# Kernel tuning notes

Hardware: AMD Instinct MI355X
Metric: run time of the kernel (lower is better)

The kernel has to match this reference:

```python
import jax, jax.numpy as jnp
import numpy as np

B, H, W = 8, 448, 448
HID, EMB, OUT = 1024, 1024, 4096
P = 12544
hgrid = wgrid = H // 14  # 32


def layernorm2d(x, wgt, bias, eps=1e-6):
    # channel-wise LN over dim 1 per spatial location, as in LayerNorm2d
    u = x.mean(1, keepdims=True)
    s = ((x - u) ** 2).mean(1, keepdims=True)
    x = (x - u) / jnp.sqrt(s + eps)
    return wgt[None, :, None, None] * x + bias[None, :, None, None]


def conv2d(x, wk, b, stride):
    y = jax.lax.conv_general_dilated(x, wk, (stride, stride), 'VALID',
                                     dimension_numbers=('NCHW', 'OIHW', 'NCHW'))
    return y + b[None, :, None, None]


def grid_sample_bilinear(feat, grid):
    # feat [B,C,h,w]; grid [B,P,2] (x,y) in [-1,1]; align_corners=False, zeros padding
    Bc, C, Hh, Ww = feat.shape
    gx = (grid[..., 0] + 1.0) * 0.5 * Ww - 0.5
    gy = (grid[..., 1] + 1.0) * 0.5 * Hh - 0.5
    x0 = jnp.floor(gx); y0 = jnp.floor(gy)
    x1 = x0 + 1.0; y1 = y0 + 1.0
    wx1 = gx - x0; wx0 = 1.0 - wx1
    wy1 = gy - y0; wy0 = 1.0 - wy1
    flat = feat.reshape(Bc, C, Hh * Ww)

    def gather(ix, iy):
        valid = (ix >= 0) & (ix < Ww) & (iy >= 0) & (iy < Hh)
        ixc = jnp.clip(ix, 0, Ww - 1).astype(jnp.int32)
        iyc = jnp.clip(iy, 0, Hh - 1).astype(jnp.int32)
        idx = iyc * Ww + ixc  # [B,P]
        g = jnp.take_along_axis(flat, idx[:, None, :], axis=2)  # [B,C,P]
        return g * valid[:, None, :].astype(g.dtype)

    return (gather(x0, y0) * (wx0 * wy0)[:, None, :]
            + gather(x1, y0) * (wx1 * wy0)[:, None, :]
            + gather(x0, y1) * (wx0 * wy1)[:, None, :]
            + gather(x1, y1) * (wx1 * wy1)[:, None, :])


def forward(images, masks, image_features, point_coords, valid_mask,
            c1w, c1b, ln1w, ln1b, c2w, c2b, ln2w, ln2b, c3w, c3b, up_w, up_b):
    x = jnp.concatenate([images, masks], axis=1)  # [B,4,H,W]
    x = conv2d(x, c1w, c1b, 7)
    x = jax.nn.gelu(layernorm2d(x, ln1w, ln1b), approximate=False)
    x = conv2d(x, c2w, c2b, 2)
    x = jax.nn.gelu(layernorm2d(x, ln2w, ln2b), approximate=False)
    x = conv2d(x, c3w, c3b, 1)  # [B,EMB,h,w]
    feat = image_features.reshape(B, hgrid, wgrid, EMB).transpose(0, 3, 1, 2)
    x = x + feat
    # point_sample: coords in [0,1], mapped to [-1,1]
    sf = grid_sample_bilinear(x, 2.0 * point_coords - 1.0)  # [B,EMB,P]
    sf = sf.transpose(0, 2, 1)  # [B,P,EMB]
    vm = valid_mask.astype(sf.dtype)
    pooled = (sf * vm[:, :, None]).sum(1) / vm.sum(1)[:, None]
    pooled = jnp.nan_to_num(pooled)
    out = pooled @ up_w.T + up_b  # [B,OUT]
    return out  # single feature level: stack([out]).mean(0) == out


def setup_inputs() -> dict:
    key = jax.random.key(0)
    ks = jax.random.split(key, 12)
    rng = np.random.default_rng(0)

    masks_np = np.zeros((B, 1, H, W), np.float32)
    coords = np.full((B, P, 2), -1.0, np.float32)
    valid = np.zeros((B, P), bool)
    for b in range(B):
        y0r = int(rng.integers(0, H // 2)); x0r = int(rng.integers(0, W // 2))
        hh = int(rng.integers(H // 4, H // 2)); ww = int(rng.integers(W // 4, W // 2))
        masks_np[b, 0, y0r:y0r + hh, x0r:x0r + ww] = 1.0
        ys, xs = np.nonzero(masks_np[b, 0])
        n = len(ys)
        sel = np.sort(rng.choice(n, size=min(P, n), replace=False))
        k = len(sel)
        coords[b, :k, 0] = xs[sel] / W  # x normalized (flip of (y,x))
        coords[b, :k, 1] = ys[sel] / H  # y normalized
        valid[b, :k] = True

    s = 0.02
    return {
        'images': jax.random.normal(ks[0], (B, 3, H, W), jnp.float32),
        'masks': jnp.asarray(masks_np),
        'image_features': jax.random.normal(ks[1], (B, hgrid * wgrid, EMB), jnp.float32),
        'point_coords': jnp.asarray(coords),
        'valid_mask': jnp.asarray(valid),
        'c1w': jax.random.normal(ks[2], (HID // 4, 4, 7, 7), jnp.float32) * s,
        'c1b': jnp.zeros((HID // 4,), jnp.float32),
        'ln1w': jnp.ones((HID // 4,), jnp.float32),
        'ln1b': jnp.zeros((HID // 4,), jnp.float32),
        'c2w': jax.random.normal(ks[3], (HID, HID // 4, 2, 2), jnp.float32) * s,
        'c2b': jnp.zeros((HID,), jnp.float32),
        'ln2w': jnp.ones((HID,), jnp.float32),
        'ln2b': jnp.zeros((HID,), jnp.float32),
        'c3w': jax.random.normal(ks[4], (EMB, HID, 1, 1), jnp.float32) * s,
        'c3b': jnp.zeros((EMB,), jnp.float32),
        'up_w': jax.random.normal(ks[5], (OUT, EMB), jnp.float32) * s,
        'up_b': jnp.zeros((OUT,), jnp.float32),
    }


def reference(images, masks, image_features, point_coords, valid_mask,
              c1w, c1b, ln1w, ln1b, c2w, c2b, ln2w, ln2b, c3w, c3b, up_w, up_b):
    return forward(images, masks, image_features, point_coords, valid_mask,
                   c1w, c1b, ln1w, ln1b, c2w, c2b, ln2w, ln2b, c3w, c3b, up_w, up_b)
```

## Files before the change

kernel.cpp:

```cpp
#include <hip/hip_runtime.h>
#include <stdint.h>

#define NB 8
#define HIN 448
#define CH1 256
#define CH2 1024
#define NLOC 1024
#define M2 8192
#define M1 32768
#define K1 224
#define NPTS 12544
#define NOUT 4096
#define CAP 384
#define MC (NB * CAP)
#define M1C (MC * 4)

typedef __attribute__((ext_vector_type(8))) short bf16x8;
typedef __attribute__((ext_vector_type(4))) float f32x4;

__device__ __forceinline__ short f2bf(float f) {
  uint32_t u = __builtin_bit_cast(uint32_t, f);
  uint32_t r = (u + 0x7fffu + ((u >> 16) & 1u)) >> 16;
  return (short)r;
}
__device__ __forceinline__ float bf2f(short s) {
  return __builtin_bit_cast(float, (uint32_t)(uint16_t)s << 16);
}
__device__ __forceinline__ float gelu_f(float x) {
  return 0.5f * x * (1.0f + erff(x * 0.70710678118654752f));
}
__device__ __forceinline__ void gload_lds16(const void* g, void* l) {
  __builtin_amdgcn_global_load_lds((const __attribute__((address_space(1))) unsigned int*)g,
                                   (__attribute__((address_space(3))) unsigned int*)l, 16, 0, 0);
}

__global__ void k_prep(const float* __restrict__ c1w, const float* __restrict__ c2w,
                       short* __restrict__ c1wb, short* __restrict__ w2p,
                       float4* __restrict__ zp, int n4) {
  int i = blockIdx.x * 256 + threadIdx.x;
  if (i < n4) zp[i] = make_float4(0.f, 0.f, 0.f, 0.f);
  if (i < CH1 * K1) {
    int o = i / K1, k = i - o * K1;
    int c = k / 56, kk = k - c * 56, r = kk >> 3, cc = kk & 7;
    c1wb[i] = f2bf(cc < 7 ? c1w[((o * 4 + c) * 7 + r) * 7 + cc] : 0.0f);
  }
  if (i < CH2 * CH2) {
    int o = i >> 10, k = i & 1023;
    int pos = k >> 8, ci = k & 255;
    w2p[i] = f2bf(c2w[(size_t)(o * 256 + ci) * 4 + pos]);
  }
}

__global__ __launch_bounds__(256) void k_pts(const float* __restrict__ coords,
                                             float* __restrict__ Aw,
                                             float* __restrict__ cnt,
                                             float* __restrict__ sumAw) {
  __shared__ float lAw[NLOC];
  __shared__ int lcnt;
  __shared__ float wsum[4];
  int t = threadIdx.x;
  int b = blockIdx.x / 49;
  int blk = blockIdx.x - b * 49;
  for (int i = t; i < NLOC; i += 256) lAw[i] = 0.f;
  if (t == 0) lcnt = 0;
  __syncthreads();
  int pi = blk * 256 + t;
  float x = coords[((size_t)b * NPTS + pi) * 2];
  float y = coords[((size_t)b * NPTS + pi) * 2 + 1];
  bool valid = (x >= 0.0f);
  if (valid) {
    float gx = x * 32.0f - 0.5f, gy = y * 32.0f - 0.5f;
    float x0f = floorf(gx), y0f = floorf(gy);
    int x0 = (int)x0f, y0 = (int)y0f;
    float wx1 = gx - x0f, wx0 = 1.0f - wx1;
    float wy1 = gy - y0f, wy0 = 1.0f - wy1;
    int xs[2] = {x0, x0 + 1}, ys[2] = {y0, y0 + 1};
    float wxs[2] = {wx0, wx1}, wys[2] = {wy0, wy1};
    #pragma unroll
    for (int cy = 0; cy < 2; cy++)
      #pragma unroll
      for (int cx = 0; cx < 2; cx++) {
        int ix = xs[cx], iy = ys[cy];
        if (ix >= 0 && ix < 32 && iy >= 0 && iy < 32)
          atomicAdd(&lAw[iy * 32 + ix], wxs[cx] * wys[cy]);
      }
  }
  unsigned long long ball = __ballot(valid);
  if ((t & 63) == 0) atomicAdd(&lcnt, (int)__popcll(ball));
  __syncthreads();
  float tsum = 0.f;
  for (int i = t; i < NLOC; i += 256) {
    float v = lAw[i];
    tsum += v;
    if (v != 0.f) atomicAdd(&Aw[b * NLOC + i], v);
  }
  #pragma unroll
  for (int m = 1; m <= 32; m <<= 1) tsum += __shfl_xor(tsum, m, 64);
  if ((t & 63) == 0) wsum[t >> 6] = tsum;
  __syncthreads();
  if (t == 0) {
    float bs = wsum[0] + wsum[1] + wsum[2] + wsum[3];
    if (bs != 0.f) atomicAdd(&sumAw[b], bs);
    if (lcnt) atomicAdd(&cnt[b], (float)lcnt);
  }
}

__global__ __launch_bounds__(256) void k_cim(const float* __restrict__ Aw,
                                             int* __restrict__ idxc,
                                             float* __restrict__ Awc,
                                             const float* __restrict__ images,
                                             const float* __restrict__ masks,
                                             short* __restrict__ A1g) {
  __shared__ float S[28 * 452];
  int t = threadIdx.x;
  if (blockIdx.x < NB) {
    int* cnts = (int*)S;
    int* offs = cnts + 256;
    int b = blockIdx.x;
    int base = b * 1024 + t * 4;
    float w[4];
    int c = 0;
    #pragma unroll
    for (int j = 0; j < 4; j++) { w[j] = Aw[base + j]; c += (w[j] != 0.f) ? 1 : 0; }
    cnts[t] = c;
    offs[t] = c;
    __syncthreads();
    for (int s = 1; s < 256; s <<= 1) {
      int v = (t >= s) ? offs[t - s] : 0;
      __syncthreads();
      offs[t] += v;
      __syncthreads();
    }
    int pos = b * CAP + offs[t] - cnts[t];
    int lim = (b + 1) * CAP;
    #pragma unroll
    for (int j = 0; j < 4; j++)
      if (w[j] != 0.f && pos < lim) { idxc[pos] = base + j; Awc[pos] = w[j]; pos++; }
    int total = offs[255];
    for (int i = total + t; i < CAP; i += 256) {
      idxc[b * CAP + i] = b * 1024;
      Awc[b * CAP + i] = 0.f;
    }
    return;
  }
  int bid = blockIdx.x - NB;
  int b = bid >> 6, y = bid & 63;
  int y7 = y * 7;
  for (int p = t; p < 3136; p += 256) {
    int row = p / 112, c4 = p - row * 112;
    int c = row / 7, r = row - c * 7;
    const float* src = (c < 3)
        ? &images[((size_t)(b * 3 + c) * 448 + y7 + r) * 448 + c4 * 4]
        : &masks[((size_t)b * 448 + y7 + r) * 448 + c4 * 4];
    *(float4*)&S[row * 452 + c4 * 4] = *(const float4*)src;
  }
  __syncthreads();
  size_t obase = (size_t)bid * 64 * K1;
  #pragma unroll
  for (int it = 0; it < 7; it++) {
    int p = it * 256 + t;
    int x = p / 28, k16 = p - x * 28;
    const float* s = &S[k16 * 452 + x * 7];
    short o[8];
    #pragma unroll
    for (int j = 0; j < 7; j++) o[j] = f2bf(s[j]);
    o[7] = 0;
    *(bf16x8*)&A1g[obase + (size_t)p * 8] = *(bf16x8*)o;
  }
}

template<int KDIM, int LDC, int MODE>
__global__ __launch_bounds__(256) void k_gemm64(
    const short* __restrict__ Amat, const int* __restrict__ idxc,
    const short* __restrict__ Bmat, const float* __restrict__ bias,
    short* __restrict__ Cout) {
  __shared__ __align__(16) char Lraw[16384];
  int t = threadIdx.x, lane = t & 63, wv = t >> 6;
  int mt0 = blockIdx.x * 64;
  int nt0 = blockIdx.y * 64;
  f32x4 acc[2][2];
  #pragma unroll
  for (int i = 0; i < 2; i++)
    #pragma unroll
    for (int j = 0; j < 2; j++) acc[i][j] = (f32x4){0.f, 0.f, 0.f, 0.f};

  int srow = lane >> 2, scol = (lane & 3) * 8;
  int wm = wv >> 1, wn = wv & 1;
  int l15 = lane & 15, lg = lane >> 4;

  int arow = mt0 + wv * 16 + srow;
  const short* Ap;
  if (MODE == 1) {
    int i = arow >> 2, pos = arow & 3;
    int loc = idxc[i];
    int b = loc >> 10, oy = (loc >> 5) & 31, ox = loc & 31;
    int yy = oy * 2 + (pos >> 1), xx = ox * 2 + (pos & 1);
    Ap = Amat + (size_t)((b * 64 + yy) * 64 + xx) * KDIM;
  } else {
    Ap = Amat + (size_t)arow * KDIM;
  }
  const short* Bp = Bmat + (size_t)(nt0 + wv * 16 + srow) * KDIM;

  auto STAGE = [&](int buf, int kt) {
    int k0 = kt * 32;
    char* As = Lraw + buf * 8192;
    char* Bs = As + 4096;
    gload_lds16(Ap + k0 + scol, As + wv * 1024);
    gload_lds16(Bp + k0 + scol, Bs + wv * 1024);
  };

  const int NT = KDIM / 32;
  STAGE(0, 0);
  __syncthreads();
  int cur = 0;
  #pragma unroll 2
  for (int kt = 0; kt < NT; kt++) {
    if (kt + 1 < NT) STAGE(cur ^ 1, kt + 1);
    const short* As = (const short*)(Lraw + cur * 8192);
    const short* Bs = As + 2048;
    bf16x8 af[2], bfr[2];
    #pragma unroll
    for (int i = 0; i < 2; i++)
      af[i] = *(const bf16x8*)&As[(wm * 32 + i * 16 + l15) * 32 + lg * 8];
    #pragma unroll
    for (int j = 0; j < 2; j++)
      bfr[j] = *(const bf16x8*)&Bs[(wn * 32 + j * 16 + l15) * 32 + lg * 8];
    #pragma unroll
    for (int i = 0; i < 2; i++)
      #pragma unroll
      for (int j = 0; j < 2; j++)
        acc[i][j] = __builtin_amdgcn_mfma_f32_16x16x32_bf16(af[i], bfr[j], acc[i][j], 0, 0, 0);
    __syncthreads();
    cur ^= 1;
  }

  short* ct = (short*)Lraw;
  #pragma unroll
  for (int i = 0; i < 2; i++)
    #pragma unroll
    for (int j = 0; j < 2; j++) {
      int cl = wn * 32 + j * 16 + l15;
      float bv = bias[nt0 + cl];
      #pragma unroll
      for (int reg = 0; reg < 4; reg++) {
        int rl = wm * 32 + i * 16 + lg * 4 + reg;
        ct[rl * 68 + cl] = f2bf(acc[i][j][reg] + bv);
      }
    }
  __syncthreads();
  #pragma unroll
  for (int it = 0; it < 2; it++) {
    int p = it * 256 + t;
    int row = p >> 3, cc = (p & 7) * 8;
    bf16x8 v = *(const bf16x8*)&ct[row * 68 + cc];
    *(bf16x8*)&Cout[(size_t)(mt0 + row) * LDC + nt0 + cc] = v;
  }
}

__global__ __launch_bounds__(256) void k_gemm2s(
    const short* __restrict__ Amat, const short* __restrict__ Bmat,
    const float* __restrict__ bias, float* __restrict__ y2p0,
    float* __restrict__ y2p1) {
  const int KDIM = 1024;
  __shared__ __align__(16) char Lraw[24576];
  int t = threadIdx.x, lane = t & 63, wv = t >> 6;
  int mt0 = blockIdx.x * 128;
  int nt0 = blockIdx.y * 64;
  int kz = blockIdx.z;
  int kbase = kz * 512;
  float* outp = kz ? y2p1 : y2p0;
  f32x4 acc[4][2];
  #pragma unroll
  for (int i = 0; i < 4; i++)
    #pragma unroll
    for (int j = 0; j < 2; j++) acc[i][j] = (f32x4){0.f, 0.f, 0.f, 0.f};

  int srow = lane >> 2, scol = (lane & 3) * 8;
  int wm = wv >> 1, wn = wv & 1;
  int l15 = lane & 15, lg = lane >> 4;
  int r0 = wv * 16, r1 = 64 + wv * 16;

  auto STAGE = [&](int buf, int kt) {
    int k0 = kbase + kt * 32;
    char* As = Lraw + buf * 12288;
    char* Bs = As + 8192;
    gload_lds16(&Amat[(size_t)(mt0 + r0 + srow) * KDIM + k0 + scol], As + r0 * 64);
    gload_lds16(&Amat[(size_t)(mt0 + r1 + srow) * KDIM + k0 + scol], As + r1 * 64);
    gload_lds16(&Bmat[(size_t)(nt0 + r0 + srow) * KDIM + k0 + scol], Bs + r0 * 64);
  };

  STAGE(0, 0);
  __syncthreads();
  int cur = 0;
  #pragma unroll 2
  for (int kt = 0; kt < 16; kt++) {
    if (kt + 1 < 16) STAGE(cur ^ 1, kt + 1);
    const short* As = (const short*)(Lraw + cur * 12288);
    const short* Bs = As + 4096;
    bf16x8 af[4], bfr[2];
    #pragma unroll
    for (int i = 0; i < 4; i++)
      af[i] = *(const bf16x8*)&As[(wm * 64 + i * 16 + l15) * 32 + lg * 8];
    #pragma unroll
    for (int j = 0; j < 2; j++)
      bfr[j] = *(const bf16x8*)&Bs[(wn * 32 + j * 16 + l15) * 32 + lg * 8];
    #pragma unroll
    for (int i = 0; i < 4; i++)
      #pragma unroll
      for (int j = 0; j < 2; j++)
        acc[i][j] = __builtin_amdgcn_mfma_f32_16x16x32_bf16(af[i], bfr[j], acc[i][j], 0, 0, 0);
    __syncthreads();
    cur ^= 1;
  }

  #pragma unroll
  for (int i = 0; i < 4; i++)
    #pragma unroll
    for (int j = 0; j < 2; j++) {
      int colg = nt0 + wn * 32 + j * 16 + l15;
      float bv = kz ? 0.0f : bias[colg];
      #pragma unroll
      for (int reg = 0; reg < 4; reg++) {
        int rowg = mt0 + wm * 64 + i * 16 + lg * 4 + reg;
        outp[(size_t)rowg * 1024 + colg] = acc[i][j][reg] + bv;
      }
    }
}

__global__ __launch_bounds__(256) void k_ln1c(const short* __restrict__ y1c,
                                              const float* __restrict__ ln1w,
                                              const float* __restrict__ ln1b,
                                              short* __restrict__ act1c) {
  int t = threadIdx.x, wv = t >> 6, lane = t & 63;
  int c = lane * 4;
  float lw[4], lb[4];
  #pragma unroll
  for (int j = 0; j < 4; j++) { lw[j] = ln1w[c + j]; lb[j] = ln1b[c + j]; }
  int j0 = blockIdx.x * 64 + wv * 16;
  for (int r = 0; r < 16; r++) {
    int j = j0 + r;
    short4 v4 = *(const short4*)&y1c[(size_t)j * 256 + c];
    float xs[4] = {bf2f(v4.x), bf2f(v4.y), bf2f(v4.z), bf2f(v4.w)};
    float s = 0.f, q = 0.f;
    #pragma unroll
    for (int jj = 0; jj < 4; jj++) { s += xs[jj]; q += xs[jj] * xs[jj]; }
    #pragma unroll
    for (int mm = 1; mm <= 32; mm <<= 1) { s += __shfl_xor(s, mm, 64); q += __shfl_xor(q, mm, 64); }
    float u = s * (1.0f / 256.0f);
    float rs = rsqrtf(q * (1.0f / 256.0f) - u * u + 1e-6f);
    short o[4];
    #pragma unroll
    for (int jj = 0; jj < 4; jj++) o[jj] = f2bf(gelu_f(lw[jj] * ((xs[jj] - u) * rs) + lb[jj]));
    *(short4*)&act1c[(size_t)j * 256 + c] = make_short4(o[0], o[1], o[2], o[3]);
  }
}

__global__ __launch_bounds__(256) void k_poolboth(
    const float* __restrict__ y2p0, const float* __restrict__ y2p1,
    const float* __restrict__ feat, const int* __restrict__ idxc,
    const float* __restrict__ ln2w, const float* __restrict__ ln2b,
    const float* __restrict__ Awc, float* __restrict__ partials,
    float* __restrict__ partialsF) {
  int t = threadIdx.x, wv = t >> 6, lane = t & 63;
  int b = blockIdx.x / 12, chunk = blockIdx.x % 12;
  int base = b * CAP + chunk * 32;
  int c0 = lane * 16;
  float lw[16], lb[16], wacc[16], facc[16];
  #pragma unroll
  for (int j = 0; j < 16; j++) {
    lw[j] = ln2w[c0 + j];
    lb[j] = ln2b[c0 + j];
    wacc[j] = 0.f;
    facc[j] = 0.f;
  }
  for (int pass = 0; pass < 8; pass++) {
    int row = base + pass * 4 + wv;
    float wt = Awc[row];
    if (wt == 0.f) continue;
    const float4* fp = (const float4*)(feat + (size_t)idxc[row] * 1024 + c0);
    #pragma unroll
    for (int j = 0; j < 4; j++) {
      float4 v = fp[j];
      facc[j * 4 + 0] += wt * v.x;
      facc[j * 4 + 1] += wt * v.y;
      facc[j * 4 + 2] += wt * v.z;
      facc[j * 4 + 3] += wt * v.w;
    }
    const float4* a0 = (const float4*)(y2p0 + (size_t)row * 1024 + c0);
    const float4* a1 = (const float4*)(y2p1 + (size_t)row * 1024 + c0);
    float xs[16];
    #pragma unroll
    for (int j = 0; j < 4; j++) {
      float4 va = a0[j], vb = a1[j];
      xs[j * 4 + 0] = va.x + vb.x;
      xs[j * 4 + 1] = va.y + vb.y;
      xs[j * 4 + 2] = va.z + vb.z;
      xs[j * 4 + 3] = va.w + vb.w;
    }
    float s = 0.f, q = 0.f;
    #pragma unroll
    for (int j = 0; j < 16; j++) { s += xs[j]; q += xs[j] * xs[j]; }
    #pragma unroll
    for (int m = 1; m <= 32; m <<= 1) { s += __shfl_xor(s, m, 64); q += __shfl_xor(q, m, 64); }
    float u = s * (1.0f / 1024.0f);
    float rs = rsqrtf(q * (1.0f / 1024.0f) - u * u + 1e-6f);
    #pragma unroll
    for (int j = 0; j < 16; j++)
      wacc[j] += wt * gelu_f(lw[j] * ((xs[j] - u) * rs) + lb[j]);
  }
  float* dst = &partials[((size_t)blockIdx.x * 4 + wv) * 1024 + c0];
  float* dstF = &partialsF[((size_t)blockIdx.x * 4 + wv) * 1024 + c0];
  #pragma unroll
  for (int j = 0; j < 4; j++) {
    *(f32x4*)&dst[j * 4] = (f32x4){wacc[j * 4], wacc[j * 4 + 1], wacc[j * 4 + 2], wacc[j * 4 + 3]};
    *(f32x4*)&dstF[j * 4] = (f32x4){facc[j * 4], facc[j * 4 + 1], facc[j * 4 + 2], facc[j * 4 + 3]};
  }
}

__global__ __launch_bounds__(256) void k_red(const float* __restrict__ partials,
                                             const float* __restrict__ partialsF,
                                             float* __restrict__ pa,
                                             float* __restrict__ pf) {
  int c = blockIdx.x * 256 + threadIdx.x;
  int b = c >> 10, ch = c & 1023;
  const float* p = partials + (size_t)(b * 48) * 1024 + ch;
  const float* pF = partialsF + (size_t)(b * 48) * 1024 + ch;
  float s = 0.f, sf = 0.f;
  #pragma unroll 8
  for (int j = 0; j < 48; j++) {
    s += p[(size_t)j * 1024];
    sf += pF[(size_t)j * 1024];
  }
  pa[c] = s;
  pf[c] = sf;
}

__global__ __launch_bounds__(256) void k_mix(const float* __restrict__ pa,
                                             const float* __restrict__ pf,
                                             const float* __restrict__ sumAw,
                                             const float* __restrict__ cnt,
                                             const float* __restrict__ c3w,
                                             const float* __restrict__ c3b,
                                             float* __restrict__ zn) {
  __shared__ float pl[8192];
  int t = threadIdx.x;
  for (int idx = t; idx < 2048; idx += 256)
    ((float4*)pl)[idx] = ((const float4*)pa)[idx];
  __syncthreads();
  int wv = t >> 6, lane = t & 63;
  int c = blockIdx.x * 4 + wv;
  float w[16];
  #pragma unroll
  for (int i = 0; i < 16; i++) w[i] = c3w[(size_t)c * 1024 + i * 64 + lane];
  float s[8];
  #pragma unroll
  for (int b = 0; b < 8; b++) s[b] = 0.f;
  #pragma unroll
  for (int i = 0; i < 16; i++) {
    int k = i * 64 + lane;
    #pragma unroll
    for (int b = 0; b < 8; b++) s[b] += w[i] * pl[b * 1024 + k];
  }
  #pragma unroll
  for (int m = 1; m <= 32; m <<= 1)
    #pragma unroll
    for (int b = 0; b < 8; b++) s[b] += __shfl_xor(s[b], m, 64);
  if (lane < 8) {
    float cv = cnt[lane];
    float z = s[lane] + sumAw[lane] * c3b[c] + pf[lane * 1024 + c];
    zn[lane * 1024 + c] = cv > 0.f ? z / cv : 0.f;
  }
}

__global__ __launch_bounds__(256) void k_out(const float* __restrict__ zn,
                                             const float* __restrict__ up_w,
                                             const float* __restrict__ up_b,
                                             float* __restrict__ out) {
  __shared__ float pl[8192];
  int t = threadIdx.x;
  for (int idx = t; idx < 2048; idx += 256)
    ((float4*)pl)[idx] = ((const float4*)zn)[idx];
  __syncthreads();
  int wv = t >> 6, lane = t & 63;
  int o = blockIdx.x * 4 + wv;
  float w[16];
  #pragma unroll
  for (int i = 0; i < 16; i++) w[i] = up_w[(size_t)o * 1024 + i * 64 + lane];
  float s[8];
  #pragma unroll
  for (int b = 0; b < 8; b++) s[b] = 0.f;
  #pragma unroll
  for (int i = 0; i < 16; i++) {
    int k = i * 64 + lane;
    #pragma unroll
    for (int b = 0; b < 8; b++) s[b] += w[i] * pl[b * 1024 + k];
  }
  #pragma unroll
  for (int m = 1; m <= 32; m <<= 1)
    #pragma unroll
    for (int b = 0; b < 8; b++) s[b] += __shfl_xor(s[b], m, 64);
  if (lane < 8) out[(size_t)lane * NOUT + o] = s[lane] + up_b[o];
}

extern "C" void kernel_launch(void* const* d_in, const int* in_sizes, int n_in,
                              void* d_out, int out_size, void* d_ws, size_t ws_size,
                              hipStream_t stream) {
  const float* images = (const float*)d_in[0];
  const float* masks  = (const float*)d_in[1];
  const float* feat   = (const float*)d_in[2];
  const float* coords = (const float*)d_in[3];
  const float* c1w  = (const float*)d_in[5];
  const float* c1b  = (const float*)d_in[6];
  const float* ln1w = (const float*)d_in[7];
  const float* ln1b = (const float*)d_in[8];
  const float* c2w  = (const float*)d_in[9];
  const float* c2b  = (const float*)d_in[10];
  const float* ln2w = (const float*)d_in[11];
  const float* ln2b = (const float*)d_in[12];
  const float* c3w  = (const float*)d_in[13];
  const float* c3b  = (const float*)d_in[14];
  const float* up_w = (const float*)d_in[15];
  const float* up_b = (const float*)d_in[16];
  float* out = (float*)d_out;

  char* ws = (char*)d_ws;
  size_t off = 0;
  auto alloc = [&](size_t bytes) -> void* {
    void* p = ws + off;
    off = (off + bytes + 255) & ~(size_t)255;
    return p;
  };
  float* Aw    = (float*)alloc(8192 * 4);
  float* cnt   = (float*)alloc(8 * 4);
  float* sumAw = (float*)alloc(8 * 4);
  size_t zeroBytes = off;
  int*   idxc  = (int*)alloc(MC * 4);
  float* Awc   = (float*)alloc(MC * 4);
  float* pa    = (float*)alloc(8192 * 4);
  float* pf    = (float*)alloc(8192 * 4);
  float* partials  = (float*)alloc((size_t)384 * 1024 * 4);
  float* partialsF = (float*)alloc((size_t)384 * 1024 * 4);
  float* zn   = (float*)alloc(8192 * 4);
  short* c1wb = (short*)alloc((size_t)CH1 * K1 * 2);
  short* w2p  = (short*)alloc((size_t)CH2 * CH2 * 2);
  short* A1g  = (short*)alloc((size_t)M1 * K1 * 2);
  short* y1c  = (short*)alloc((size_t)M1C * 256 * 2);
  short* act1c = (short*)alloc((size_t)MC * 1024 * 2);
  float* y2p0 = (float*)alloc((size_t)MC * 1024 * 4);
  float* y2p1 = (float*)alloc((size_t)MC * 1024 * 4);

  int n4 = (int)(zeroBytes / 16);
  k_prep<<<4096, 256, 0, stream>>>(c1w, c2w, c1wb, w2p, (float4*)d_ws, n4);
  k_pts<<<NB * 49, 256, 0, stream>>>(coords, Aw, cnt, sumAw);
  k_cim<<<NB + 512, 256, 0, stream>>>(Aw, idxc, Awc, images, masks, A1g);
  k_gemm64<K1, 256, 1><<<dim3(M1C / 64, 4), 256, 0, stream>>>(A1g, idxc, c1wb, c1b, y1c);
  k_ln1c<<<M1C / 64, 256, 0, stream>>>(y1c, ln1w, ln1b, act1c);
  k_gemm2s<<<dim3(MC / 128, 16, 2), 256, 0, stream>>>(act1c, w2p, c2b, y2p0, y2p1);
  k_poolboth<<<96, 256, 0, stream>>>(y2p0, y2p1, feat, idxc, ln2w, ln2b, Awc, partials, partialsF);
  k_red<<<32, 256, 0, stream>>>(partials, partialsF, pa, pf);
  k_mix<<<256, 256, 0, stream>>>(pa, pf, sumAw, cnt, c3w, c3b, zn);
  k_out<<<NOUT / 4, 256, 0, stream>>>(zn, up_w, up_b, out);
}
```

Measured before the change: 111.1 us.

## Build im2col only for sampled locations and swizzle conv2 GEMM block order

The im2col step used to convert the whole 448x448 input for every location. It now builds patches only for the compacted set of sampled locations, in a new kernel that reads idxc. Compaction becomes its own kernel launched first, and the first GEMM drops its indirect row addressing because it now reads a dense compacted A matrix. Separately, the conv2 split-K GEMM uses a 1D grid with a block-index swizzle across XCD-like groups of 8, which should improve L2 locality. The cost is one extra kernel launch and a serialized dependency of im2col on compaction.

```diff
diff --git a/kernel.cpp b/kernel.cpp
--- a/kernel.cpp
+++ b/kernel.cpp
@@ -105,75 +105,86 @@
   }
 }
 
-__global__ __launch_bounds__(256) void k_cim(const float* __restrict__ Aw,
-                                             int* __restrict__ idxc,
-                                             float* __restrict__ Awc,
+__global__ __launch_bounds__(256) void k_compact(const float* __restrict__ Aw,
+                                                 int* __restrict__ idxc,
+                                                 float* __restrict__ Awc) {
+  __shared__ int cnts[256], offs[256];
+  int t = threadIdx.x, b = blockIdx.x;
+  int base = b * 1024 + t * 4;
+  float w[4];
+  int c = 0;
+  #pragma unroll
+  for (int j = 0; j < 4; j++) { w[j] = Aw[base + j]; c += (w[j] != 0.f) ? 1 : 0; }
+  cnts[t] = c;
+  offs[t] = c;
+  __syncthreads();
+  for (int s = 1; s < 256; s <<= 1) {
+    int v = (t >= s) ? offs[t - s] : 0;
+    __syncthreads();
+    offs[t] += v;
+    __syncthreads();
+  }
+  int pos = b * CAP + offs[t] - cnts[t];
+  int lim = (b + 1) * CAP;
+  #pragma unroll
+  for (int j = 0; j < 4; j++)
+    if (w[j] != 0.f && pos < lim) { idxc[pos] = base + j; Awc[pos] = w[j]; pos++; }
+  int total = offs[255];
+  for (int i = total + t; i < CAP; i += 256) {
+    idxc[b * CAP + i] = b * 1024;
+    Awc[b * CAP + i] = 0.f;
+  }
+}
+
+__global__ __launch_bounds__(256) void k_imc(const int* __restrict__ idxc,
                                              const float* __restrict__ images,
                                              const float* __restrict__ masks,
-                                             short* __restrict__ A1g) {
-  __shared__ float S[28 * 452];
+                                             short* __restrict__ A1c) {
+  __shared__ short ct[64 * K1];
   int t = threadIdx.x;
-  if (blockIdx.x < NB) {
-    int* cnts = (int*)S;
-    int* offs = cnts + 256;
-    int b = blockIdx.x;
-    int base = b * 1024 + t * 4;
-    float w[4];
-    int c = 0;
-    #pragma unroll
-    for (int j = 0; j < 4; j++) { w[j] = Aw[base + j]; c += (w[j] != 0.f) ? 1 : 0; }
-    cnts[t] = c;
-    offs[t] = c;
-    __syncthreads();
-    for (int s = 1; s < 256; s <<= 1) {
-      int v = (t >= s) ? offs[t - s] : 0;
-      __syncthreads();
-      offs[t] += v;
-      __syncthreads();
+  int i0 = blockIdx.x * 16;
+  int loc = t >> 4;
+  int rem = t & 15;
+  int c = rem >> 2, kh = (rem >> 1) & 1, rh = rem & 1;
+  int gi = idxc[i0 + loc];
+  int b = gi >> 10, oy = (gi >> 5) & 31, ox = gi & 31;
+  int yy = oy * 2 + kh;
+  int xbase = ox * 14;
+  int r0 = rh * 4, rn = rh ? 3 : 4;
+  const float* plane = (c < 3)
+      ? images + (size_t)(b * 3 + c) * 448 * 448
+      : masks + (size_t)b * 448 * 448;
+  for (int rr = 0; rr < rn; rr++) {
+    int r = r0 + rr;
+    const float* src = plane + (size_t)(yy * 7 + r) * 448 + xbase;
+    short tmp[14];
+    #pragma unroll
+    for (int p = 0; p < 7; p++) {
+      float2 v = *(const float2*)&src[p * 2];
+      tmp[p * 2] = f2bf(v.x);
+      tmp[p * 2 + 1] = f2bf(v.y);
     }
-    int pos = b * CAP + offs[t] - cnts[t];
-    int lim = (b + 1) * CAP;
-    #pragma unroll
-    for (int j = 0; j < 4; j++)
-      if (w[j] != 0.f && pos < lim) { idxc[pos] = base + j; Awc[pos] = w[j]; pos++; }
-    int total = offs[255];
-    for (int i = total + t; i < CAP; i += 256) {
-      idxc[b * CAP + i] = b * 1024;
-      Awc[b * CAP + i] = 0.f;
+    #pragma unroll
+    for (int kw = 0; kw < 2; kw++) {
+      short* dst = &ct[(loc * 4 + kh * 2 + kw) * K1 + c * 56 + r * 8];
+      #pragma unroll
+      for (int cc = 0; cc < 7; cc++) dst[cc] = tmp[kw * 7 + cc];
+      dst[7] = 0;
     }
-    return;
-  }
-  int bid = blockIdx.x - NB;
-  int b = bid >> 6, y = bid & 63;
-  int y7 = y * 7;
-  for (int p = t; p < 3136; p += 256) {
-    int row = p / 112, c4 = p - row * 112;
-    int c = row / 7, r = row - c * 7;
-    const float* src = (c < 3)
-        ? &images[((size_t)(b * 3 + c) * 448 + y7 + r) * 448 + c4 * 4]
-        : &masks[((size_t)b * 448 + y7 + r) * 448 + c4 * 4];
-    *(float4*)&S[row * 452 + c4 * 4] = *(const float4*)src;
-  }
-  __syncthreads();
-  size_t obase = (size_t)bid * 64 * K1;
+  }
+  __syncthreads();
+  size_t obase = (size_t)blockIdx.x * 64 * K1;
   #pragma unroll
   for (int it = 0; it < 7; it++) {
     int p = it * 256 + t;
-    int x = p / 28, k16 = p - x * 28;
-    const float* s = &S[k16 * 452 + x * 7];
-    short o[8];
-    #pragma unroll
-    for (int j = 0; j < 7; j++) o[j] = f2bf(s[j]);
-    o[7] = 0;
-    *(bf16x8*)&A1g[obase + (size_t)p * 8] = *(bf16x8*)o;
-  }
-}
-
-template<int KDIM, int LDC, int MODE>
+    *(bf16x8*)&A1c[obase + (size_t)p * 8] = *(const bf16x8*)&ct[p * 8];
+  }
+}
+
+template<int KDIM, int LDC>
 __global__ __launch_bounds__(256) void k_gemm64(
-    const short* __restrict__ Amat, const int* __restrict__ idxc,
-    const short* __restrict__ Bmat, const float* __restrict__ bias,
-    short* __restrict__ Cout) {
+    const short* __restrict__ Amat, const short* __restrict__ Bmat,
+    const float* __restrict__ bias, short* __restrict__ Cout) {
   __shared__ __align__(16) char Lraw[16384];
   int t = threadIdx.x, lane = t & 63, wv = t >> 6;
   int mt0 = blockIdx.x * 64;
@@ -188,17 +199,7 @@
   int wm = wv >> 1, wn = wv & 1;
   int l15 = lane & 15, lg = lane >> 4;
 
-  int arow = mt0 + wv * 16 + srow;
-  const short* Ap;
-  if (MODE == 1) {
-    int i = arow >> 2, pos = arow & 3;
-    int loc = idxc[i];
-    int b = loc >> 10, oy = (loc >> 5) & 31, ox = loc & 31;
-    int yy = oy * 2 + (pos >> 1), xx = ox * 2 + (pos & 1);
-    Ap = Amat + (size_t)((b * 64 + yy) * 64 + xx) * KDIM;
-  } else {
-    Ap = Amat + (size_t)arow * KDIM;
-  }
+  const short* Ap = Amat + (size_t)(mt0 + wv * 16 + srow) * KDIM;
   const short* Bp = Bmat + (size_t)(nt0 + wv * 16 + srow) * KDIM;
 
   auto STAGE = [&](int buf, int kt) {
@@ -264,9 +265,13 @@
   const int KDIM = 1024;
   __shared__ __align__(16) char Lraw[24576];
   int t = threadIdx.x, lane = t & 63, wv = t >> 6;
-  int mt0 = blockIdx.x * 128;
-  int nt0 = blockIdx.y * 64;
-  int kz = blockIdx.z;
+  int swz = (blockIdx.x & 7) * 96 + (blockIdx.x >> 3);
+  int kz = swz / 384;
+  int rem = swz - kz * 384;
+  int by = rem / 24;
+  int bx = rem - by * 24;
+  int mt0 = bx * 128;
+  int nt0 = by * 64;
   int kbase = kz * 512;
   float* outp = kz ? y2p1 : y2p0;
   f32x4 acc[4][2];
@@ -543,7 +548,7 @@
   float* zn   = (float*)alloc(8192 * 4);
   short* c1wb = (short*)alloc((size_t)CH1 * K1 * 2);
   short* w2p  = (short*)alloc((size_t)CH2 * CH2 * 2);
-  short* A1g  = (short*)alloc((size_t)M1 * K1 * 2);
+  short* A1c  = (short*)alloc((size_t)M1C * K1 * 2);
   short* y1c  = (short*)alloc((size_t)M1C * 256 * 2);
   short* act1c = (short*)alloc((size_t)MC * 1024 * 2);
   float* y2p0 = (float*)alloc((size_t)MC * 1024 * 4);
@@ -552,10 +557,11 @@
   int n4 = (int)(zeroBytes / 16);
   k_prep<<<4096, 256, 0, stream>>>(c1w, c2w, c1wb, w2p, (float4*)d_ws, n4);
   k_pts<<<NB * 49, 256, 0, stream>>>(coords, Aw, cnt, sumAw);
-  k_cim<<<NB + 512, 256, 0, stream>>>(Aw, idxc, Awc, images, masks, A1g);
-  k_gemm64<K1, 256, 1><<<dim3(M1C / 64, 4), 256, 0, stream>>>(A1g, idxc, c1wb, c1b, y1c);
+  k_compact<<<NB, 256, 0, stream>>>(Aw, idxc, Awc);
+  k_imc<<<MC / 16, 256, 0, stream>>>(idxc, images, masks, A1c);
+  k_gemm64<K1, 256><<<dim3(M1C / 64, 4), 256, 0, stream>>>(A1c, c1wb, c1b, y1c);
   k_ln1c<<<M1C / 64, 256, 0, stream>>>(y1c, ln1w, ln1b, act1c);
-  k_gemm2s<<<dim3(MC / 128, 16, 2), 256, 0, stream>>>(act1c, w2p, c2b, y2p0, y2p1);
+  k_gemm2s<<<768, 256, 0, stream>>>(act1c, w2p, c2b, y2p0, y2p1);
   k_poolboth<<<96, 256, 0, stream>>>(y2p0, y2p1, feat, idxc, ln2w, ln2b, Awc, partials, partialsF);
   k_red<<<32, 256, 0, stream>>>(partials, partialsF, pa, pf);
   k_mix<<<256, 256, 0, stream>>>(pa, pf, sumAw, cnt, c3w, c3b, zn);
```

Result: no change. 110.3 us (-0.8%).
